# Performance work log

Measured on AMD Instinct MI355X. Metric: run time of the kernel, lower is better.

The kernel has to match this reference:

```python
import jax, jax.numpy as jnp
import numpy as np

D_MODEL = 1024
N_HEADS = 16
D_K = D_MODEL // N_HEADS


def setup_inputs() -> dict:
    key = jax.random.key(0)
    ks = jax.random.split(key, 7)
    B, S = 2, 2048
    q = jax.random.normal(ks[0], (B, S, D_MODEL), dtype=jnp.float32)
    k = jax.random.normal(ks[1], (B, S, D_MODEL), dtype=jnp.float32)
    v = jax.random.normal(ks[2], (B, S, D_MODEL), dtype=jnp.float32)
    mask = jnp.ones((B, 1, S, S), dtype=bool)
    scale = 1.0 / np.sqrt(D_MODEL)
    w_q = jax.random.normal(ks[3], (D_MODEL, D_MODEL), dtype=jnp.float32) * scale
    w_k = jax.random.normal(ks[4], (D_MODEL, D_MODEL), dtype=jnp.float32) * scale
    w_v = jax.random.normal(ks[5], (D_MODEL, D_MODEL), dtype=jnp.float32) * scale
    w_o = jax.random.normal(ks[6], (D_MODEL, D_MODEL), dtype=jnp.float32) * scale
    return {"q": q, "k": k, "v": v, "mask": mask,
            "w_q": w_q, "w_k": w_k, "w_v": w_v, "w_o": w_o}


def reference(q, k, v, mask, w_q, w_k, w_v, w_o):
    B, S, _ = q.shape
    # projections (nn.Linear: x @ W^T, no bias)
    def split_heads(x):  # [B,S,D] -> [B,H,S,d_k]
        return x.reshape(B, -1, N_HEADS, D_K).transpose(0, 2, 1, 3)
    query = split_heads(q @ w_q.T)
    key_h = split_heads(k @ w_k.T)
    value = split_heads(v @ w_v.T)
    # naive scaled dot-product attention: full [B,H,S,S] scores materialized
    scores = jnp.einsum('bhqd,bhkd->bhqk', query, key_h) / jnp.sqrt(
        jnp.asarray(D_K, query.dtype))
    scores = jnp.where(mask, scores, jnp.asarray(-1e9, scores.dtype))
    attn = jax.nn.softmax(scores, axis=-1)  # dropout p=0.0 -> identity
    x = jnp.einsum('bhqk,bhkd->bhqd', attn, value)
    x = x.transpose(0, 2, 1, 3).reshape(B, S, N_HEADS * D_K)
    return x @ w_o.T
```

## Files before the change

kernel.cpp:

```cpp
#include <hip/hip_runtime.h>
#include <hip/hip_bf16.h>
#include <math.h>

typedef __bf16 bf16;
typedef __bf16 bf16x8 __attribute__((ext_vector_type(8)));
typedef float f32x4 __attribute__((ext_vector_type(4)));
typedef float f32x16 __attribute__((ext_vector_type(16)));
typedef unsigned u32x4 __attribute__((ext_vector_type(4)));

#define MFMA16(a, b, c) __builtin_amdgcn_mfma_f32_16x16x32_bf16((a), (b), (c), 0, 0, 0)
#define MFMA32(a, b, c) __builtin_amdgcn_mfma_f32_32x32x16_bf16((a), (b), (c), 0, 0, 0)

__device__ __forceinline__ void gl_lds16(const void* g, void* l) {
    __builtin_amdgcn_global_load_lds(
        (__attribute__((address_space(1))) void*)(g),
        (__attribute__((address_space(3))) void*)(l),
        16, 0, 0);
}

__device__ __forceinline__ unsigned cvt_pk_bf16(float lo, float hi) {
    unsigned r;
    asm("v_cvt_pk_bf16_f32 %0, %1, %2" : "=v"(r) : "v"(lo), "v"(hi));
    return r;
}

__global__ __launch_bounds__(256) void cvt7(
    const float* __restrict__ w0, const float* __restrict__ w1,
    const float* __restrict__ w2, const float* __restrict__ w3,
    const float* __restrict__ x0, const float* __restrict__ x1,
    const float* __restrict__ x2, bf16* __restrict__ dst) {
    const int z = blockIdx.y;
    const float* src;
    bf16* out;
    if (z < 4) {
        if (blockIdx.x >= 512) return;
        src = (z == 0) ? w0 : (z == 1) ? w1 : (z == 2) ? w2 : w3;
        out = dst + (size_t)z * 1048576;
    } else {
        src = (z == 4) ? x0 : (z == 5) ? x1 : x2;
        out = dst + 4 * 1048576 + (size_t)(z - 4) * 4194304;
    }
    const int i = (blockIdx.x * 256 + threadIdx.x) * 8;
    float4 a = ((const float4*)(src + i))[0];
    float4 b = ((const float4*)(src + i))[1];
    bf16x8 o;
    o[0] = (bf16)a.x; o[1] = (bf16)a.y; o[2] = (bf16)a.z; o[3] = (bf16)a.w;
    o[4] = (bf16)b.x; o[5] = (bf16)b.y; o[6] = (bf16)b.z; o[7] = (bf16)b.w;
    *(bf16x8*)(out + i) = o;
}

template <int EP>
__device__ __forceinline__ void gemm_bf(const bf16* __restrict__ A,
                                        const bf16* __restrict__ B,
                                        void* __restrict__ Cv,
                                        const int m0, const int n0) {
    constexpr int K = 1024;
    __shared__ __align__(16) bf16 As[128 * 32];
    __shared__ __align__(16) bf16 Bs[128 * 32];

    const int t = threadIdx.x;
    const int lane = t & 63;
    const int w = t >> 6;
    const int wm = (w & 1) * 64;
    const int wn = (w >> 1) * 64;
    const int lr = lane & 15;
    const int lq8 = (lane >> 4) * 8;
    const int rq = (lane >> 4) * 4;

    f32x4 acc[4][4] = {};

    const int srow = t >> 2;
    const int sch = (t & 3) * 8;
    char* lA = (char*)As;
    char* lB = (char*)Bs;

    for (int k0 = 0; k0 < K; k0 += 32) {
        gl_lds16(A + (size_t)(m0 + srow) * K + k0 + sch,      lA + t * 16);
        gl_lds16(A + (size_t)(m0 + 64 + srow) * K + k0 + sch, lA + 4096 + t * 16);
        gl_lds16(B + (size_t)(n0 + srow) * K + k0 + sch,      lB + t * 16);
        gl_lds16(B + (size_t)(n0 + 64 + srow) * K + k0 + sch, lB + 4096 + t * 16);
        __syncthreads();

        bf16x8 af[4], bfr[4];
#pragma unroll
        for (int i = 0; i < 4; ++i) {
            af[i]  = *(const bf16x8*)&As[(wm + i * 16 + lr) * 32 + lq8];
            bfr[i] = *(const bf16x8*)&Bs[(wn + i * 16 + lr) * 32 + lq8];
        }
#pragma unroll
        for (int mi = 0; mi < 4; ++mi)
#pragma unroll
            for (int ni = 0; ni < 4; ++ni)
                acc[mi][ni] = MFMA16(af[mi], bfr[ni], acc[mi][ni]);
        __syncthreads();
    }

#pragma unroll
    for (int mi = 0; mi < 4; ++mi) {
#pragma unroll
        for (int ni = 0; ni < 4; ++ni) {
#pragma unroll
            for (int r = 0; r < 4; ++r) {
                const int m = m0 + wm + mi * 16 + rq + r;
                const int n = n0 + wn + ni * 16 + lr;
                const float vv = acc[mi][ni][r];
                if constexpr (EP == 0) {
                    bf16* C = (bf16*)Cv;
                    const int b = m >> 11, s = m & 2047;
                    const int h = n >> 6,  d = n & 63;
                    C[(((size_t)(b * 16 + h)) * 2048 + s) * 64 + d] = (bf16)vv;
                } else if constexpr (EP == 1) {
                    float* C = (float*)Cv;
                    C[(size_t)m * 1024 + n] = vv;
                } else {
                    bf16* C = (bf16*)Cv;
                    C[((size_t)(n >> 11) * 1024 + m) * 2048 + (n & 2047)] = (bf16)vv;
                }
            }
        }
    }
}

__global__ __launch_bounds__(256, 3) void qkv_bf(
    const bf16* __restrict__ Xq, const bf16* __restrict__ Xk,
    const bf16* __restrict__ Xv, const bf16* __restrict__ Wc,
    bf16* __restrict__ Qb, bf16* __restrict__ Kb, bf16* __restrict__ Vb) {
    const int z = blockIdx.z;
    if (z == 0)
        gemm_bf<0>(Xq, Wc, Qb, blockIdx.x * 128, blockIdx.y * 128);
    else if (z == 1)
        gemm_bf<0>(Xk, Wc + 1048576, Kb, blockIdx.x * 128, blockIdx.y * 128);
    else
        gemm_bf<2>(Wc + 2 * 1048576, Xv, Vb, blockIdx.y * 128, blockIdx.x * 128);
}

__global__ __launch_bounds__(256, 2) void out_gemm(
    const bf16* __restrict__ X, const bf16* __restrict__ W, float* __restrict__ C) {
    gemm_bf<1>(X, W, C, blockIdx.x * 128, blockIdx.y * 128);
}

template <int MODE>
__device__ __forceinline__ void gemm_f32tok(const void* __restrict__ Av,
                                            const void* __restrict__ Bv,
                                            bf16* __restrict__ C,
                                            const int m0, const int n0) {
    constexpr int K = 1024;
    __shared__ __align__(16) bf16 As[128 * 32];
    __shared__ __align__(16) bf16 Bs[128 * 32];

    const int t = threadIdx.x;
    const int lane = t & 63;
    const int w = t >> 6;
    const int wm = (w & 1) * 64;
    const int wn = (w >> 1) * 64;
    const int lr = lane & 15;
    const int lq8 = (lane >> 4) * 8;
    const int rq = (lane >> 4) * 4;

    f32x4 acc[4][4] = {};
    const int srow = t >> 2;
    const int sch = (t & 3) * 8;
    const int ar = t >> 1;
    const int ac = (t & 1) * 16;
    char* lA = (char*)As;
    char* lB = (char*)Bs;

    for (int k0 = 0; k0 < K; k0 += 32) {
        if constexpr (MODE == 0) {
            const float* X = (const float*)Av;
            const float* p = X + (size_t)(m0 + ar) * K + k0 + ac;
            float4 f0 = ((const float4*)p)[0], f1 = ((const float4*)p)[1];
            float4 f2 = ((const float4*)p)[2], f3 = ((const float4*)p)[3];
            bf16x8 o0, o1;
            o0[0]=(bf16)f0.x; o0[1]=(bf16)f0.y; o0[2]=(bf16)f0.z; o0[3]=(bf16)f0.w;
            o0[4]=(bf16)f1.x; o0[5]=(bf16)f1.y; o0[6]=(bf16)f1.z; o0[7]=(bf16)f1.w;
            o1[0]=(bf16)f2.x; o1[1]=(bf16)f2.y; o1[2]=(bf16)f2.z; o1[3]=(bf16)f2.w;
            o1[4]=(bf16)f3.x; o1[5]=(bf16)f3.y; o1[6]=(bf16)f3.z; o1[7]=(bf16)f3.w;
            *(bf16x8*)&As[ar * 32 + ac]     = o0;
            *(bf16x8*)&As[ar * 32 + ac + 8] = o1;
        } else {
            const bf16* X = (const bf16*)Av;
            gl_lds16(X + (size_t)(m0 + srow) * K + k0 + sch,      lA + t * 16);
            gl_lds16(X + (size_t)(m0 + 64 + srow) * K + k0 + sch, lA + 4096 + t * 16);
        }
        if constexpr (MODE == 2) {
            const float* X = (const float*)Bv;
            const float* p = X + (size_t)(n0 + ar) * K + k0 + ac;
            float4 f0 = ((const float4*)p)[0], f1 = ((const float4*)p)[1];
            float4 f2 = ((const float4*)p)[2], f3 = ((const float4*)p)[3];
            bf16x8 o0, o1;
            o0[0]=(bf16)f0.x; o0[1]=(bf16)f0.y; o0[2]=(bf16)f0.z; o0[3]=(bf16)f0.w;
            o0[4]=(bf16)f1.x; o0[5]=(bf16)f1.y; o0[6]=(bf16)f1.z; o0[7]=(bf16)f1.w;
            o1[0]=(bf16)f2.x; o1[1]=(bf16)f2.y; o1[2]=(bf16)f2.z; o1[3]=(bf16)f2.w;
            o1[4]=(bf16)f3.x; o1[5]=(bf16)f3.y; o1[6]=(bf16)f3.z; o1[7]=(bf16)f3.w;
            *(bf16x8*)&Bs[ar * 32 + ac]     = o0;
            *(bf16x8*)&Bs[ar * 32 + ac + 8] = o1;
        } else {
            const bf16* W = (const bf16*)Bv;
            gl_lds16(W + (size_t)(n0 + srow) * K + k0 + sch,      lB + t * 16);
            gl_lds16(W + (size_t)(n0 + 64 + srow) * K + k0 + sch, lB + 4096 + t * 16);
        }
        __syncthreads();

        bf16x8 af[4], bfr[4];
#pragma unroll
        for (int i = 0; i < 4; ++i) {
            af[i]  = *(const bf16x8*)&As[(wm + i * 16 + lr) * 32 + lq8];
            bfr[i] = *(const bf16x8*)&Bs[(wn + i * 16 + lr) * 32 + lq8];
        }
#pragma unroll
        for (int mi = 0; mi < 4; ++mi)
#pragma unroll
            for (int ni = 0; ni < 4; ++ni)
                acc[mi][ni] = MFMA16(af[mi], bfr[ni], acc[mi][ni]);
        __syncthreads();
    }

#pragma unroll
    for (int mi = 0; mi < 4; ++mi) {
#pragma unroll
        for (int ni = 0; ni < 4; ++ni) {
#pragma unroll
            for (int r = 0; r < 4; ++r) {
                const int m = m0 + wm + mi * 16 + rq + r;
                const int n = n0 + wn + ni * 16 + lr;
                const float vv = acc[mi][ni][r];
                if constexpr (MODE == 0) {
                    const int b = m >> 11, s = m & 2047;
                    const int h = n >> 6,  d = n & 63;
                    C[(((size_t)(b * 16 + h)) * 2048 + s) * 64 + d] = (bf16)vv;
                } else {
                    C[((size_t)(n >> 11) * 1024 + m) * 2048 + (n & 2047)] = (bf16)vv;
                }
            }
        }
    }
}

__global__ __launch_bounds__(256, 2) void qkv_f32(
    const float* __restrict__ q, const float* __restrict__ k, const float* __restrict__ v,
    const bf16* __restrict__ Wc, bf16* __restrict__ Qb, bf16* __restrict__ Kb,
    bf16* __restrict__ Vb) {
    const int z = blockIdx.z;
    if (z == 0)
        gemm_f32tok<0>(q, Wc, Qb, blockIdx.x * 128, blockIdx.y * 128);
    else if (z == 1)
        gemm_f32tok<0>(k, Wc + 1048576, Kb, blockIdx.x * 128, blockIdx.y * 128);
    else
        gemm_f32tok<2>(Wc + 2 * 1048576, v, Vb, blockIdx.y * 128, blockIdx.x * 128);
}

__global__ __launch_bounds__(512, 4) void attn_kernel(
    const bf16* __restrict__ Qb, const bf16* __restrict__ Kb,
    const bf16* __restrict__ Vb, bf16* __restrict__ Xb) {
    constexpr int S = 2048;

    __shared__ __align__(16) bf16 smem[17408];

    const int t = threadIdx.x;
    const int lane = t & 63;
    const int w = t >> 6;
    const int wg = w & 3;
    const int kh = w >> 2;
    const int l31 = lane & 31;
    const int half = lane >> 5;

    const int lin = blockIdx.x;
    const int g = lin >> 3;
    const int bh = (lin & 7) + 8 * (g & 3);
    const int q0 = (g >> 2) * 128 + wg * 32;

    const bf16* Q  = Qb + (size_t)bh * S * 64;
    const bf16* Kh = Kb + (size_t)bh * S * 64;
    const bf16* Vh = Vb + (size_t)bh * 64 * S;

    const float qscale = 0.125f * 1.4426950408889634f;
    bf16x8 qf[4];
#pragma unroll
    for (int c = 0; c < 4; ++c) {
        bf16x8 v0 = *(const bf16x8*)(Q + (size_t)(q0 + l31) * 64 + c * 16 + half * 8);
#pragma unroll
        for (int e = 0; e < 8; ++e) v0[e] = (bf16)((float)v0[e] * qscale);
        qf[c] = v0;
    }

    f32x16 od[2] = {};
    float ls0 = 0.f, ls1 = 0.f, ls2 = 0.f, ls3 = 0.f;

    const int tt = t & 255;
    const int sr = tt >> 2;
    const int sc = (tt & 3) * 2;
    const bf16* pKg = Kh + ((size_t)kh * 1024 + sr) * 64 + sc * 8;
    const bf16* pVg = Vh + (size_t)sr * S + kh * 1024 + sc * 8;
    bf16* KsH = smem + kh * 4096;
    bf16* VsH = smem + 8192 + kh * 4096;
    int wKo[2];
#pragma unroll
    for (int c = 0; c < 2; ++c)
        wKo[c] = (sr >> 1) * 128 + ((((sr & 1) << 3) + sc + c) ^ ((sr >> 1) & 15)) * 8;

    bf16x8 pk[2], pv[2];
#pragma unroll
    for (int c = 0; c < 2; ++c) {
        pk[c] = *(const bf16x8*)(pKg + c * 8);
        pv[c] = *(const bf16x8*)(pVg + c * 8);
    }

    const int fbase = (l31 >> 1) * 128;
    const int fb8 = (l31 & 1) << 3;
    const int fsw = l31 >> 1;

    for (int j = 0; j < 16; ++j) {
        __syncthreads();
#pragma unroll
        for (int c = 0; c < 2; ++c) {
            *(bf16x8*)&KsH[wKo[c]] = pk[c];
            *(bf16x8*)&VsH[wKo[c]] = pv[c];
        }
        __syncthreads();

        f32x16 sacc[2] = {};
#pragma unroll
        for (int kt = 0; kt < 2; ++kt) {
#pragma unroll
            for (int c = 0; c < 4; ++c) {
                bf16x8 kf = *(const bf16x8*)
                    &KsH[kt * 2048 + fbase + ((fb8 + c * 2 + half) ^ fsw) * 8];
                sacc[kt] = MFMA32(kf, qf[c], sacc[kt]);
            }
        }

        if (j + 1 < 16) {
            pKg += 4096;
            pVg += 64;
#pragma unroll
            for (int c = 0; c < 2; ++c) {
                pk[c] = *(const bf16x8*)(pKg + c * 8);
                pv[c] = *(const bf16x8*)(pVg + c * 8);
            }
        }

#pragma unroll
        for (int kt = 0; kt < 2; ++kt) {
            float ex[16];
#pragma unroll
            for (int r = 0; r < 16; ++r)
                ex[r] = exp2f(sacc[kt][r]);
            ls0 += ex[0] + ex[4] + ex[8]  + ex[12];
            ls1 += ex[1] + ex[5] + ex[9]  + ex[13];
            ls2 += ex[2] + ex[6] + ex[10] + ex[14];
            ls3 += ex[3] + ex[7] + ex[11] + ex[15];

            unsigned pa[8];
#pragma unroll
            for (int c2 = 0; c2 < 2; ++c2) {
#pragma unroll
                for (int wd = 0; wd < 2; ++wd) {
                    unsigned x = cvt_pk_bf16(ex[c2 * 8 + wd * 2 + 0], ex[c2 * 8 + wd * 2 + 1]);
                    unsigned y = cvt_pk_bf16(ex[c2 * 8 + wd * 2 + 4], ex[c2 * 8 + wd * 2 + 5]);
                    asm("v_permlane32_swap_b32 %0, %1" : "+v"(x), "+v"(y));
                    pa[c2 * 4 + wd]     = x;
                    pa[c2 * 4 + wd + 2] = y;
                }
            }

#pragma unroll
            for (int c2 = 0; c2 < 2; ++c2) {
                u32x4 aw;
                aw[0] = pa[c2 * 4 + 0]; aw[1] = pa[c2 * 4 + 1];
                aw[2] = pa[c2 * 4 + 2]; aw[3] = pa[c2 * 4 + 3];
                bf16x8 ap = __builtin_bit_cast(bf16x8, aw);
#pragma unroll
                for (int dt = 0; dt < 2; ++dt) {
                    const int cgv = kt * 4 + c2 * 2 + half;
                    bf16x8 vf = *(const bf16x8*)
                        &VsH[dt * 2048 + fbase + ((fb8 + cgv) ^ fsw) * 8];
                    od[dt] = MFMA32(ap, vf, od[dt]);
                }
            }
        }
    }

    float lsum = ls0 + ls1 + ls2 + ls3;
    float ltot = lsum + __shfl_xor(lsum, 32);

    __syncthreads();
    float* fsm = (float*)smem;
    const int so = (wg * 64 + lane) * 34;
    if (kh == 1) {
        fsm[so + 32] = ltot;
#pragma unroll
        for (int r = 0; r < 16; ++r) {
            fsm[so + r]      = od[0][r];
            fsm[so + 16 + r] = od[1][r];
        }
    }
    __syncthreads();
    if (kh == 0) {
        ltot += fsm[so + 32];
        const float inv = 1.f / fmaxf(ltot, 1e-30f);
        const int b = bh >> 4, hh = bh & 15;
#pragma unroll
        for (int r = 0; r < 16; ++r) {
            const int qrow = (r & 3) + 8 * (r >> 2) + 4 * half;
            const float invr = __shfl(inv, qrow);
            const size_t base = ((size_t)(b * 2048 + q0 + qrow)) * 1024 + hh * 64;
            Xb[base + l31]      = (bf16)((od[0][r] + fsm[so + r]) * invr);
            Xb[base + 32 + l31] = (bf16)((od[1][r] + fsm[so + 16 + r]) * invr);
        }
    }
}

extern "C" void kernel_launch(void* const* d_in, const int* in_sizes, int n_in,
                              void* d_out, int out_size, void* d_ws, size_t ws_size,
                              hipStream_t stream) {
    const float* q  = (const float*)d_in[0];
    const float* k  = (const float*)d_in[1];
    const float* v  = (const float*)d_in[2];
    const float* wq = (const float*)d_in[4];
    const float* wk = (const float*)d_in[5];
    const float* wv = (const float*)d_in[6];
    const float* wo = (const float*)d_in[7];
    float* out = (float*)d_out;

    const bool big = ws_size >= (size_t)64 * 1024 * 1024;
    bf16* Wc = (bf16*)d_ws;
    const dim3 blk(256);

    if (big) {
        bf16* Xq = Wc + 4 * 1048576;
        bf16* Xk = Xq + 4194304;
        bf16* Xv = Xk + 4194304;
        bf16* Qb = Xv + 4194304;
        bf16* Kb = Qb + 4194304;
        bf16* Vb = Kb + 4194304;
        bf16* Xb = Vb + 4194304;
        cvt7<<<dim3(2048, 7), blk, 0, stream>>>(wq, wk, wv, wo, q, k, v, Wc);
        qkv_bf<<<dim3(32, 8, 3), blk, 0, stream>>>(Xq, Xk, Xv, Wc, Qb, Kb, Vb);
        attn_kernel<<<dim3(512), dim3(512), 0, stream>>>(Qb, Kb, Vb, Xb);
        out_gemm<<<dim3(32, 8), blk, 0, stream>>>(Xb, Wc + 3 * 1048576, out);
    } else {
        bf16* Qb = Wc + 4 * 1048576;
        bf16* Kb = Qb + 4194304;
        bf16* Vb = Kb + 4194304;
        bf16* Xb = Vb + 4194304;
        cvt7<<<dim3(512, 4), blk, 0, stream>>>(wq, wk, wv, wo, q, k, v, Wc);
        qkv_f32<<<dim3(32, 8, 3), blk, 0, stream>>>(q, k, v, Wc, Qb, Kb, Vb);
        attn_kernel<<<dim3(512), dim3(512), 0, stream>>>(Qb, Kb, Vb, Xb);
        out_gemm<<<dim3(32, 8), blk, 0, stream>>>(Xb, Wc + 3 * 1048576, out);
    }
}
```

Measured before the change: 237.9 us.

## Deepen GEMM K-tile, widen out_gemm to 512 threads, prioritize attention MFMAs

The shared bf16 GEMM now stages a 64-wide K slice per iteration instead of 32, which halves the barrier and loop overhead per unit of work. The output projection gets its own 512-thread kernel with eight waves each computing a 64x32 sub-tile, giving more waves per block. The attention kernel also raises wave priority around its MFMA sections with s_setprio so matrix work is issued ahead of the exp/convert code in other waves. Costs: double the LDS per block and a row stride of 64 bf16 with no swizzle, which may cause LDS bank conflicts, plus lower per-wave reuse in out_gemm.

```diff
diff --git a/kernel.cpp b/kernel.cpp
--- a/kernel.cpp
+++ b/kernel.cpp
@@ -55,8 +55,8 @@
                                         void* __restrict__ Cv,
                                         const int m0, const int n0) {
     constexpr int K = 1024;
-    __shared__ __align__(16) bf16 As[128 * 32];
-    __shared__ __align__(16) bf16 Bs[128 * 32];
+    __shared__ __align__(16) bf16 As[128 * 64];
+    __shared__ __align__(16) bf16 Bs[128 * 64];
 
     const int t = threadIdx.x;
     const int lane = t & 63;
@@ -69,29 +69,33 @@
 
     f32x4 acc[4][4] = {};
 
-    const int srow = t >> 2;
-    const int sch = (t & 3) * 8;
+    const int srow = t >> 3;
+    const int sch = (t & 7) * 8;
     char* lA = (char*)As;
     char* lB = (char*)Bs;
 
-    for (int k0 = 0; k0 < K; k0 += 32) {
-        gl_lds16(A + (size_t)(m0 + srow) * K + k0 + sch,      lA + t * 16);
-        gl_lds16(A + (size_t)(m0 + 64 + srow) * K + k0 + sch, lA + 4096 + t * 16);
-        gl_lds16(B + (size_t)(n0 + srow) * K + k0 + sch,      lB + t * 16);
-        gl_lds16(B + (size_t)(n0 + 64 + srow) * K + k0 + sch, lB + 4096 + t * 16);
-        __syncthreads();
-
-        bf16x8 af[4], bfr[4];
+    for (int k0 = 0; k0 < K; k0 += 64) {
 #pragma unroll
         for (int i = 0; i < 4; ++i) {
-            af[i]  = *(const bf16x8*)&As[(wm + i * 16 + lr) * 32 + lq8];
-            bfr[i] = *(const bf16x8*)&Bs[(wn + i * 16 + lr) * 32 + lq8];
-        }
-#pragma unroll
-        for (int mi = 0; mi < 4; ++mi)
-#pragma unroll
-            for (int ni = 0; ni < 4; ++ni)
-                acc[mi][ni] = MFMA16(af[mi], bfr[ni], acc[mi][ni]);
+            gl_lds16(A + (size_t)(m0 + i * 32 + srow) * K + k0 + sch, lA + i * 4096 + t * 16);
+            gl_lds16(B + (size_t)(n0 + i * 32 + srow) * K + k0 + sch, lB + i * 4096 + t * 16);
+        }
+        __syncthreads();
+
+#pragma unroll
+        for (int kk = 0; kk < 64; kk += 32) {
+            bf16x8 af[4], bfr[4];
+#pragma unroll
+            for (int i = 0; i < 4; ++i) {
+                af[i]  = *(const bf16x8*)&As[(wm + i * 16 + lr) * 64 + kk + lq8];
+                bfr[i] = *(const bf16x8*)&Bs[(wn + i * 16 + lr) * 64 + kk + lq8];
+            }
+#pragma unroll
+            for (int mi = 0; mi < 4; ++mi)
+#pragma unroll
+                for (int ni = 0; ni < 4; ++ni)
+                    acc[mi][ni] = MFMA16(af[mi], bfr[ni], acc[mi][ni]);
+        }
         __syncthreads();
     }
 
@@ -134,9 +138,65 @@
         gemm_bf<2>(Wc + 2 * 1048576, Xv, Vb, blockIdx.y * 128, blockIdx.x * 128);
 }
 
-__global__ __launch_bounds__(256, 2) void out_gemm(
+__global__ __launch_bounds__(512, 2) void out_gemm(
     const bf16* __restrict__ X, const bf16* __restrict__ W, float* __restrict__ C) {
-    gemm_bf<1>(X, W, C, blockIdx.x * 128, blockIdx.y * 128);
+    constexpr int K = 1024;
+    __shared__ __align__(16) bf16 As[128 * 64];
+    __shared__ __align__(16) bf16 Bs[128 * 64];
+
+    const int t = threadIdx.x;
+    const int lane = t & 63;
+    const int w = t >> 6;
+    const int wm = (w >> 2) * 64;
+    const int wn = (w & 3) * 32;
+    const int lr = lane & 15;
+    const int lq8 = (lane >> 4) * 8;
+    const int rq = (lane >> 4) * 4;
+    const int m0 = blockIdx.x * 128, n0 = blockIdx.y * 128;
+
+    f32x4 acc[4][2] = {};
+
+    const int srow = t >> 3;
+    const int sch = (t & 7) * 8;
+    char* lA = (char*)As;
+    char* lB = (char*)Bs;
+
+    for (int k0 = 0; k0 < K; k0 += 64) {
+#pragma unroll
+        for (int i = 0; i < 2; ++i) {
+            gl_lds16(X + (size_t)(m0 + i * 64 + srow) * K + k0 + sch, lA + i * 8192 + t * 16);
+            gl_lds16(W + (size_t)(n0 + i * 64 + srow) * K + k0 + sch, lB + i * 8192 + t * 16);
+        }
+        __syncthreads();
+
+#pragma unroll
+        for (int kk = 0; kk < 64; kk += 32) {
+            bf16x8 af[4], bfr[2];
+#pragma unroll
+            for (int i = 0; i < 4; ++i)
+                af[i] = *(const bf16x8*)&As[(wm + i * 16 + lr) * 64 + kk + lq8];
+#pragma unroll
+            for (int i = 0; i < 2; ++i)
+                bfr[i] = *(const bf16x8*)&Bs[(wn + i * 16 + lr) * 64 + kk + lq8];
+#pragma unroll
+            for (int mi = 0; mi < 4; ++mi)
+#pragma unroll
+                for (int ni = 0; ni < 2; ++ni)
+                    acc[mi][ni] = MFMA16(af[mi], bfr[ni], acc[mi][ni]);
+        }
+        __syncthreads();
+    }
+
+#pragma unroll
+    for (int mi = 0; mi < 4; ++mi)
+#pragma unroll
+        for (int ni = 0; ni < 2; ++ni)
+#pragma unroll
+            for (int r = 0; r < 4; ++r) {
+                const int m = m0 + wm + mi * 16 + rq + r;
+                const int n = n0 + wn + ni * 16 + lr;
+                C[(size_t)m * 1024 + n] = acc[mi][ni][r];
+            }
 }
 
 template <int MODE>
@@ -320,6 +380,7 @@
         __syncthreads();
 
         f32x16 sacc[2] = {};
+        __builtin_amdgcn_s_setprio(1);
 #pragma unroll
         for (int kt = 0; kt < 2; ++kt) {
 #pragma unroll
@@ -329,6 +390,7 @@
                 sacc[kt] = MFMA32(kf, qf[c], sacc[kt]);
             }
         }
+        __builtin_amdgcn_s_setprio(0);
 
         if (j + 1 < 16) {
             pKg += 4096;
@@ -364,6 +426,7 @@
                 }
             }
 
+            __builtin_amdgcn_s_setprio(1);
 #pragma unroll
             for (int c2 = 0; c2 < 2; ++c2) {
                 u32x4 aw;
@@ -378,6 +441,7 @@
                     od[dt] = MFMA32(ap, vf, od[dt]);
                 }
             }
+            __builtin_amdgcn_s_setprio(0);
         }
     }
 
@@ -438,7 +502,7 @@
         cvt7<<<dim3(2048, 7), blk, 0, stream>>>(wq, wk, wv, wo, q, k, v, Wc);
         qkv_bf<<<dim3(32, 8, 3), blk, 0, stream>>>(Xq, Xk, Xv, Wc, Qb, Kb, Vb);
         attn_kernel<<<dim3(512), dim3(512), 0, stream>>>(Qb, Kb, Vb, Xb);
-        out_gemm<<<dim3(32, 8), blk, 0, stream>>>(Xb, Wc + 3 * 1048576, out);
+        out_gemm<<<dim3(32, 8), dim3(512), 0, stream>>>(Xb, Wc + 3 * 1048576, out);
     } else {
         bf16* Qb = Wc + 4 * 1048576;
         bf16* Kb = Qb + 4194304;
@@ -447,6 +511,6 @@
         cvt7<<<dim3(512, 4), blk, 0, stream>>>(wq, wk, wv, wo, q, k, v, Wc);
         qkv_f32<<<dim3(32, 8, 3), blk, 0, stream>>>(q, k, v, Wc, Qb, Kb, Vb);
         attn_kernel<<<dim3(512), dim3(512), 0, stream>>>(Qb, Kb, Vb, Xb);
-        out_gemm<<<dim3(32, 8), blk, 0, stream>>>(Xb, Wc + 3 * 1048576, out);
-    }
-}
+        out_gemm<<<dim3(32, 8), dim3(512), 0, stream>>>(Xb, Wc + 3 * 1048576, out);
+    }
+}
```

After: 267.6 us. +12.5%, slower.
